# Kernel tuning notes

Measured on AMD Instinct MI355X. Metric: run time of the kernel, lower is better.

The kernel has to match this reference:

```python
import jax, jax.numpy as jnp
import numpy as np

B, S, D = 2, 4096, 256
H, DH, DM = 8, 32, 1024
ROPE_BASE = 10000.0
LN_EPS = 1e-5


def _layer_norm(x, g, b):
    mu = jnp.mean(x, axis=-1, keepdims=True)
    var = jnp.mean(jnp.square(x - mu), axis=-1, keepdims=True)
    return (x - mu) * jax.lax.rsqrt(var + LN_EPS) * g + b


def _rope(x):
    # x: [b, s, h, d_head]; lucidrains interleaved-pair RoPE
    s, d = x.shape[1], x.shape[-1]
    inv_freq = 1.0 / (ROPE_BASE ** (jnp.arange(0, d, 2, dtype=jnp.float32) / d))  # [d/2]
    freqs = jnp.arange(s, dtype=jnp.float32)[:, None] * inv_freq[None, :]          # [s, d/2]
    freqs = jnp.repeat(freqs, 2, axis=-1)                                          # [s, d]
    cos = jnp.cos(freqs)[None, :, None, :]
    sin = jnp.sin(freqs)[None, :, None, :]
    x1, x2 = x[..., 0::2], x[..., 1::2]
    rot = jnp.stack((-x2, x1), axis=-1).reshape(x.shape)
    return x * cos + rot * sin


def setup_inputs() -> dict:
    key = jax.random.key(0)
    ks = jax.random.split(key, 8)
    sw = 1.0 / np.sqrt(D)
    return {
        "x": jax.random.normal(ks[0], (B, S, D), jnp.float32),
        "Wq": jax.random.normal(ks[1], (D, D), jnp.float32) * sw,
        "Wk": jax.random.normal(ks[2], (D, D), jnp.float32) * sw,
        "Wv": jax.random.normal(ks[3], (D, D), jnp.float32) * sw,
        "Wo": jax.random.normal(ks[4], (D, D), jnp.float32) * sw,
        "ln1_g": jnp.ones((D,), jnp.float32),
        "ln1_b": jnp.zeros((D,), jnp.float32),
        "ln2_g": jnp.ones((D,), jnp.float32),
        "ln2_b": jnp.zeros((D,), jnp.float32),
        "W2": jax.random.normal(ks[5], (DM, D), jnp.float32) * sw,
        "b2": jnp.zeros((DM,), jnp.float32),
        "W3": jax.random.normal(ks[6], (D, DM), jnp.float32) * (1.0 / np.sqrt(DM)),
        "b3": jnp.zeros((D,), jnp.float32),
    }


def reference(x, Wq, Wk, Wv, Wo, ln1_g, ln1_b, ln2_g, ln2_b, W2, b2, W3, b3):
    b, s, d = x.shape
    h, dh = H, DH
    xn = _layer_norm(x, ln1_g, ln1_b)
    q = (xn @ Wq.T).reshape(b, s, h, dh)
    k = (xn @ Wk.T).reshape(b, s, h, dh)
    v = (xn @ Wv.T).reshape(b, s, h, dh)
    q = _rope(q)
    k = _rope(k)
    # scores: [b, h, q, k] (full matrix, matching original implementation)
    scores = jnp.einsum('bqhd,bkhd->bhqk', q, k) / np.sqrt(dh)
    attn = jax.nn.softmax(scores, axis=-1)
    out = jnp.einsum('bhqk,bkhd->bqhd', attn, v).reshape(b, s, d)
    out = out @ Wo.T
    mlp_in = out + x
    y = _layer_norm(mlp_in, ln2_g, ln2_b)
    y = jax.nn.gelu(y @ W2.T + b2, approximate=False)
    y = y @ W3.T + b3
    return y + mlp_in
```

## Files before the change

### kernel.cpp

```cpp
#include <hip/hip_runtime.h>
#include <math.h>

#define D 256
#define S 4096
#define H 8
#define DH 32
#define DM 1024
#define NTOK 8192

typedef __attribute__((ext_vector_type(8))) short short8;
typedef __attribute__((ext_vector_type(4))) float f32x4;

#define QSCALE (0.17677669529663687f * 1.4426950408889634f)

__device__ inline unsigned short f2bf(float f) {
    union { float f; unsigned u; } v; v.f = f;
    unsigned r = v.u + 0x7fffu + ((v.u >> 16) & 1u);
    return (unsigned short)(r >> 16);
}
__device__ inline void gload16(const void* g, void* l) {
    __builtin_amdgcn_global_load_lds((const __attribute__((address_space(1))) void*)g,
                                     (__attribute__((address_space(3))) void*)l, 16, 0, 0);
}

__global__ void conv_all(const float* __restrict__ Wq, const float* __restrict__ Wk,
                         const float* __restrict__ Wv, const float* __restrict__ Wo,
                         const float* __restrict__ W2, const float* __restrict__ W3,
                         unsigned short* __restrict__ wqkv, unsigned short* __restrict__ wo_b,
                         unsigned short* __restrict__ w2_b, unsigned short* __restrict__ w3_b,
                         float* __restrict__ ct, float* __restrict__ st) {
    int i = blockIdx.x * 256 + threadIdx.x;
    if (i < 196608) {
        const float* s = (i < 65536) ? Wq : ((i < 131072) ? Wk : Wv);
        wqkv[i] = f2bf(s[i & 65535]);
    } else if (i < 262144) {
        wo_b[i - 196608] = f2bf(Wo[i - 196608]);
    } else if (i < 524288) {
        w2_b[i - 262144] = f2bf(W2[i - 262144]);
    } else if (i < 786432) {
        w3_b[i - 524288] = f2bf(W3[i - 524288]);
    } else {
        int j = i - 786432;
        int spos = j >> 4, pi = j & 15;
        float inv_freq = powf(10000.0f, -(float)(2 * pi) / 32.0f);
        float fr = (float)spos * inv_freq;
        ct[j] = cosf(fr);
        st[j] = sinf(fr);
    }
}

__global__ void ln_kernel(const float* __restrict__ x, const float* __restrict__ g,
                          const float* __restrict__ b, unsigned short* __restrict__ out) {
    __shared__ float red[8];
    int row = blockIdx.x;
    int tid = threadIdx.x;
    float v = x[(size_t)row * D + tid];
    float s = v, s2 = v * v;
    #pragma unroll
    for (int off = 32; off > 0; off >>= 1) {
        s  += __shfl_xor(s, off, 64);
        s2 += __shfl_xor(s2, off, 64);
    }
    int wave = tid >> 6;
    if ((tid & 63) == 0) { red[wave] = s; red[wave + 4] = s2; }
    __syncthreads();
    float sum   = red[0] + red[1] + red[2] + red[3];
    float sumsq = red[4] + red[5] + red[6] + red[7];
    float mu  = sum * (1.0f / D);
    float var = sumsq * (1.0f / D) - mu * mu;
    float rs  = rsqrtf(var + 1e-5f);
    out[(size_t)row * D + tid] = f2bf((v - mu) * rs * g[tid] + b[tid]);
}

__global__ __launch_bounds__(256) void gemm_fat(const unsigned short* __restrict__ A,
        const unsigned short* __restrict__ Bw, void* __restrict__ outp,
        unsigned short* __restrict__ vt,
        const float* __restrict__ bias, const float* __restrict__ res,
        const float* __restrict__ ct, const float* __restrict__ st,
        int N, int K, int mode) {
    __shared__ unsigned short As[64 * 256];
    __shared__ unsigned short Bs[64 * 256];
    int tid = threadIdx.x;
    int w = tid >> 6, l = tid & 63;
    int lm = l & 15, lg = l >> 4;
    int wm = (w >> 1) * 32, wn = (w & 1) * 32;
    int bm = blockIdx.x * 64, bn = blockIdx.y * 64;
    int row0 = tid >> 5, pc = tid & 31;
    int pcx = (pc ^ (row0 & 7)) * 8;
    const int swz = lm & 7;
    f32x4 acc[2][2] = {};

    for (int kp = 0; kp < K; kp += 256) {
        if (kp) __syncthreads();
        const unsigned short* Ag = A + (size_t)(bm + row0) * K + kp + pcx;
        const unsigned short* Bg = Bw + (size_t)(bn + row0) * K + kp + pcx;
        unsigned short* al = &As[w * 512];
        unsigned short* bl = &Bs[w * 512];
        #pragma unroll
        for (int it = 0; it < 8; ++it) {
            gload16(Ag + (size_t)it * 8 * K, al + it * 2048);
            gload16(Bg + (size_t)it * 8 * K, bl + it * 2048);
        }
        __syncthreads();
        #pragma unroll
        for (int kk = 0; kk < 8; ++kk) {
            short8 af[2], bf[2];
            int ch = ((kk * 4 + lg) ^ swz) * 8;
            #pragma unroll
            for (int i = 0; i < 2; ++i) af[i] = *(const short8*)&As[(wm + i * 16 + lm) * 256 + ch];
            #pragma unroll
            for (int i = 0; i < 2; ++i) bf[i] = *(const short8*)&Bs[(wn + i * 16 + lm) * 256 + ch];
            #pragma unroll
            for (int mi = 0; mi < 2; ++mi)
                #pragma unroll
                for (int ni = 0; ni < 2; ++ni)
                    acc[mi][ni] = __builtin_amdgcn_mfma_f32_16x16x32_bf16(af[mi], bf[ni], acc[mi][ni], 0, 0, 0);
        }
    }

    if (mode == 0) {
        if (bn >= 512) {
            #pragma unroll
            for (int mi = 0; mi < 2; ++mi) {
                #pragma unroll
                for (int ni = 0; ni < 2; ++ni) {
                    int ng = bn + wn + ni * 16 + lm - 512;
                    int hh = ng >> 5, dh = ng & 31;
                    int mg0 = bm + wm + mi * 16 + lg * 4;
                    int bb = mg0 >> 12, ss = mg0 & 4095;
                    ushort4 pv;
                    pv.x = f2bf(acc[mi][ni][0]); pv.y = f2bf(acc[mi][ni][1]);
                    pv.z = f2bf(acc[mi][ni][2]); pv.w = f2bf(acc[mi][ni][3]);
                    *(ushort4*)(vt + ((size_t)((bb * 8 + hh) * 32 + dh)) * S + ss) = pv;
                }
            }
        } else {
            #pragma unroll
            for (int mi = 0; mi < 2; ++mi) {
                #pragma unroll
                for (int ni = 0; ni < 2; ++ni) {
                    int ng = bn + wn + ni * 16 + lm;
                    int pi = (ng & 31) >> 1;
                    float sgn = (ng & 1) ? 1.f : -1.f;
                    float qs  = (ng < 256) ? QSCALE : 1.f;
                    #pragma unroll
                    for (int r2 = 0; r2 < 4; ++r2) {
                        int mg = bm + wm + mi * 16 + lg * 4 + r2;
                        int spos = mg & (S - 1);
                        float vv = acc[mi][ni][r2];
                        float pv = __shfl_xor(vv, 1, 64);
                        float cs = ct[spos * 16 + pi];
                        float sn = st[spos * 16 + pi];
                        float ov = (vv * cs + sgn * pv * sn) * qs;
                        ((unsigned short*)outp)[(size_t)mg * N + ng] = f2bf(ov);
                    }
                }
            }
        }
        return;
    }
    #pragma unroll
    for (int mi = 0; mi < 2; ++mi) {
        #pragma unroll
        for (int ni = 0; ni < 2; ++ni) {
            int ng = bn + wn + ni * 16 + lm;
            #pragma unroll
            for (int r2 = 0; r2 < 4; ++r2) {
                int mg = bm + wm + mi * 16 + lg * 4 + r2;
                float v = acc[mi][ni][r2];
                size_t idx = (size_t)mg * N + ng;
                if (mode == 1) {
                    ((float*)outp)[idx] = v + res[idx];
                } else if (mode == 2) {
                    float t = v + bias[ng];
                    ((unsigned short*)outp)[idx] = f2bf(0.5f * t * (1.0f + erff(t * 0.70710678118654752f)));
                } else {
                    ((float*)outp)[idx] = v + bias[ng] + res[idx];
                }
            }
        }
    }
}

__global__ __launch_bounds__(512) void attn_kernel(const unsigned short* __restrict__ Cq,
        const unsigned short* __restrict__ vt, unsigned short* __restrict__ out) {
    __shared__ unsigned short Ks[2][64][32];
    __shared__ unsigned short Vs[2][32][64];
    __shared__ unsigned short Ones[16][64];
    int tid = threadIdx.x;
    int w = tid >> 6, l = tid & 63;
    int lm = l & 15, lg = l >> 4;
    int qt = blockIdx.x & 31;
    int bh = blockIdx.x >> 5;
    int b = bh >> 3, h = bh & 7;
    int q0 = qt * 128 + w * 16;

    if (tid < 256) {
        unsigned short val = (tid < 16) ? (unsigned short)0x3F80 : (unsigned short)0;
        *(ushort4*)(&Ones[0][0] + tid * 4) = make_ushort4(val, val, val, val);
    }

    const short8 qf = *(const short8*)(Cq + ((size_t)(b * S + q0 + lm)) * 768 + h * DH + lg * 8);
    int ws = w & 3;
    int p = ws * 16 + (l >> 2);
    int krow = ((p >> 5) << 5) + (((p >> 2) & 3) << 3) + (((p >> 4) & 1) << 2) + (p & 3);
    const unsigned short* kg = Cq + ((size_t)(b * S)) * 768 + 256 + h * 32
                               + (size_t)krow * 768 + ((l & 3) ^ ((l >> 3) & 3)) * 8;
    const unsigned short* vg = vt + ((size_t)(bh * 32 + ws * 8 + (l >> 3))) * S + ((l & 7) ^ (l >> 3)) * 8;
    unsigned short* klds0 = &Ks[0][ws * 16][0];
    unsigned short* vlds0 = &Vs[0][ws * 8][0];
    unsigned short* klds1 = &Ks[1][ws * 16][0];
    unsigned short* vlds1 = &Vs[1][ws * 8][0];
    const int kswz = (lm >> 1) & 3;
    const int vswz = lm & 7;

    f32x4 o0 = {0.f, 0.f, 0.f, 0.f}, o1 = {0.f, 0.f, 0.f, 0.f}, o2 = {0.f, 0.f, 0.f, 0.f};
    const f32x4 z = {0.f, 0.f, 0.f, 0.f};

    if (w < 4) gload16(kg, klds0);
    else       gload16(vg, vlds0);

    #pragma unroll 2
    for (int it = 0; it < S / 64; ++it) {
        int cur = it & 1;
        __syncthreads();
        if (it + 1 < S / 64) {
            if (w < 4) gload16(kg + (size_t)(it + 1) * 64 * 768, cur ? klds0 : klds1);
            else       gload16(vg + (size_t)(it + 1) * 64,       cur ? vlds0 : vlds1);
        }
        #pragma unroll
        for (int half = 0; half < 2; ++half) {
            short8 kf0 = *(const short8*)&Ks[cur][half * 32 + lm][(lg ^ kswz) * 8];
            short8 kf1 = *(const short8*)&Ks[cur][half * 32 + 16 + lm][(lg ^ kswz) * 8];
            f32x4 s0 = __builtin_amdgcn_mfma_f32_16x16x32_bf16(kf0, qf, z, 0, 0, 0);
            f32x4 s1 = __builtin_amdgcn_mfma_f32_16x16x32_bf16(kf1, qf, z, 0, 0, 0);
            unsigned u0[4], u1[4];
            #pragma unroll
            for (int i = 0; i < 4; ++i) {
                union { float f; unsigned u; } c0, c1;
                c0.f = __builtin_amdgcn_exp2f(s0[i]);
                c1.f = __builtin_amdgcn_exp2f(s1[i]);
                u0[i] = c0.u;
                u1[i] = c1.u;
            }
            union { unsigned u[4]; short8 s; } pk;
            pk.u[0] = __builtin_amdgcn_perm(u0[1], u0[0], 0x07060302u);
            pk.u[1] = __builtin_amdgcn_perm(u0[3], u0[2], 0x07060302u);
            pk.u[2] = __builtin_amdgcn_perm(u1[1], u1[0], 0x07060302u);
            pk.u[3] = __builtin_amdgcn_perm(u1[3], u1[2], 0x07060302u);
            short8 pf = pk.s;
            int vc = ((half * 4 + lg) ^ vswz) * 8;
            short8 va0 = *(const short8*)&Vs[cur][lm][vc];
            short8 va1 = *(const short8*)&Vs[cur][16 + lm][vc];
            short8 va2 = *(const short8*)&Ones[lm][vc];
            o0 = __builtin_amdgcn_mfma_f32_16x16x32_bf16(va0, pf, o0, 0, 0, 0);
            o1 = __builtin_amdgcn_mfma_f32_16x16x32_bf16(va1, pf, o1, 0, 0, 0);
            o2 = __builtin_amdgcn_mfma_f32_16x16x32_bf16(va2, pf, o2, 0, 0, 0);
        }
    }
    float lsum = __shfl(o2[0], lm, 64);
    float inv = 1.0f / lsum;
    ushort4 r0, r1;
    r0.x = f2bf(o0[0] * inv); r0.y = f2bf(o0[1] * inv);
    r0.z = f2bf(o0[2] * inv); r0.w = f2bf(o0[3] * inv);
    r1.x = f2bf(o1[0] * inv); r1.y = f2bf(o1[1] * inv);
    r1.z = f2bf(o1[2] * inv); r1.w = f2bf(o1[3] * inv);
    unsigned short* ob = out + ((size_t)(b * S + q0 + lm)) * D + h * DH;
    *(ushort4*)(ob + lg * 4)      = r0;
    *(ushort4*)(ob + 16 + lg * 4) = r1;
}

extern "C" void kernel_launch(void* const* d_in, const int* in_sizes, int n_in,
                              void* d_out, int out_size, void* d_ws, size_t ws_size,
                              hipStream_t stream) {
    const float* x     = (const float*)d_in[0];
    const float* Wq    = (const float*)d_in[1];
    const float* Wk    = (const float*)d_in[2];
    const float* Wv    = (const float*)d_in[3];
    const float* Wo    = (const float*)d_in[4];
    const float* ln1_g = (const float*)d_in[5];
    const float* ln1_b = (const float*)d_in[6];
    const float* ln2_g = (const float*)d_in[7];
    const float* ln2_b = (const float*)d_in[8];
    const float* W2    = (const float*)d_in[9];
    const float* b2    = (const float*)d_in[10];
    const float* W3    = (const float*)d_in[11];
    const float* b3    = (const float*)d_in[12];

    char* w8 = (char*)d_ws;
    unsigned short* wqkv = (unsigned short*)(w8);
    unsigned short* wo_b = (unsigned short*)(w8 + 393216);
    unsigned short* w2_b = (unsigned short*)(w8 + 524288);
    unsigned short* w3_b = (unsigned short*)(w8 + 1048576);
    float*          ct   = (float*)(w8 + 1572864);
    float*          st   = (float*)(w8 + 1835008);
    unsigned short* xn   = (unsigned short*)(w8 + 2097152);
    unsigned short* Cq   = (unsigned short*)(w8 + 6291456);
    unsigned short* hb   = Cq;
    unsigned short* vtb  = (unsigned short*)(w8 + 23068672);
    unsigned short* ab   = (unsigned short*)(w8 + 27262976);
    float*          mlpin= (float*)(w8 + 31457280);
    unsigned short* yn   = xn;

    conv_all<<<3328, 256, 0, stream>>>(Wq, Wk, Wv, Wo, W2, W3, wqkv, wo_b, w2_b, w3_b, ct, st);
    ln_kernel<<<NTOK, 256, 0, stream>>>(x, ln1_g, ln1_b, xn);
    gemm_fat<<<dim3(128, 12), 256, 0, stream>>>(xn, wqkv, Cq, vtb, nullptr, nullptr, ct, st, 768, 256, 0);
    attn_kernel<<<512, 512, 0, stream>>>(Cq, vtb, ab);
    gemm_fat<<<dim3(128, 4), 256, 0, stream>>>(ab, wo_b, mlpin, nullptr, nullptr, x, nullptr, nullptr, 256, 256, 1);
    ln_kernel<<<NTOK, 256, 0, stream>>>(mlpin, ln2_g, ln2_b, yn);
    gemm_fat<<<dim3(128, 16), 256, 0, stream>>>(yn, w2_b, hb, nullptr, b2, nullptr, nullptr, nullptr, 1024, 256, 2);
    gemm_fat<<<dim3(128, 4), 256, 0, stream>>>(hb, w3_b, (float*)d_out, nullptr, b3, mlpin, nullptr, nullptr, 256, 1024, 3);
}
```

Measured before the change: 206.2 us.

## Split attention keys across two wave groups and load GEMM weights into registers

The attention kernel now gives 64 queries to each block and splits the key range between two groups of four waves. Each group double-buffers its own K/V tiles, and the partial outputs and denominators are combined through shared memory at the end. This doubles the block count to 1024, for more parallelism and fewer sequential iterations per wave. Separately, the GEMM loads B-operand fragments straight from global memory into registers instead of staging them in LDS. This halves LDS use, but adds register pressure and uncoalesced-ish global loads.

```diff
diff --git a/kernel.cpp b/kernel.cpp
--- a/kernel.cpp
+++ b/kernel.cpp
@@ -72,14 +72,13 @@
     out[(size_t)row * D + tid] = f2bf((v - mu) * rs * g[tid] + b[tid]);
 }
 
-__global__ __launch_bounds__(256) void gemm_fat(const unsigned short* __restrict__ A,
+__global__ __launch_bounds__(256) void gemm3(const unsigned short* __restrict__ A,
         const unsigned short* __restrict__ Bw, void* __restrict__ outp,
         unsigned short* __restrict__ vt,
         const float* __restrict__ bias, const float* __restrict__ res,
         const float* __restrict__ ct, const float* __restrict__ st,
         int N, int K, int mode) {
     __shared__ unsigned short As[64 * 256];
-    __shared__ unsigned short Bs[64 * 256];
     int tid = threadIdx.x;
     int w = tid >> 6, l = tid & 63;
     int lm = l & 15, lg = l >> 4;
@@ -93,28 +92,30 @@
     for (int kp = 0; kp < K; kp += 256) {
         if (kp) __syncthreads();
         const unsigned short* Ag = A + (size_t)(bm + row0) * K + kp + pcx;
-        const unsigned short* Bg = Bw + (size_t)(bn + row0) * K + kp + pcx;
         unsigned short* al = &As[w * 512];
-        unsigned short* bl = &Bs[w * 512];
-        #pragma unroll
-        for (int it = 0; it < 8; ++it) {
+        #pragma unroll
+        for (int it = 0; it < 8; ++it)
             gload16(Ag + (size_t)it * 8 * K, al + it * 2048);
-            gload16(Bg + (size_t)it * 8 * K, bl + it * 2048);
-        }
+        short8 breg[2][8];
+        const unsigned short* Bg = Bw + (size_t)(bn + wn + lm) * K + kp + lg * 8;
+        #pragma unroll
+        for (int ni = 0; ni < 2; ++ni)
+            #pragma unroll
+            for (int kk = 0; kk < 8; ++kk)
+                breg[ni][kk] = *(const short8*)(Bg + (size_t)(ni * 16) * K + kk * 32);
         __syncthreads();
         #pragma unroll
         for (int kk = 0; kk < 8; ++kk) {
-            short8 af[2], bf[2];
+            short8 af[2];
             int ch = ((kk * 4 + lg) ^ swz) * 8;
             #pragma unroll
-            for (int i = 0; i < 2; ++i) af[i] = *(const short8*)&As[(wm + i * 16 + lm) * 256 + ch];
-            #pragma unroll
-            for (int i = 0; i < 2; ++i) bf[i] = *(const short8*)&Bs[(wn + i * 16 + lm) * 256 + ch];
+            for (int i = 0; i < 2; ++i)
+                af[i] = *(const short8*)&As[(wm + i * 16 + lm) * 256 + ch];
             #pragma unroll
             for (int mi = 0; mi < 2; ++mi)
                 #pragma unroll
                 for (int ni = 0; ni < 2; ++ni)
-                    acc[mi][ni] = __builtin_amdgcn_mfma_f32_16x16x32_bf16(af[mi], bf[ni], acc[mi][ni], 0, 0, 0);
+                    acc[mi][ni] = __builtin_amdgcn_mfma_f32_16x16x32_bf16(af[mi], breg[ni][kk], acc[mi][ni], 0, 0, 0);
         }
     }
 
@@ -184,54 +185,51 @@
 
 __global__ __launch_bounds__(512) void attn_kernel(const unsigned short* __restrict__ Cq,
         const unsigned short* __restrict__ vt, unsigned short* __restrict__ out) {
-    __shared__ unsigned short Ks[2][64][32];
-    __shared__ unsigned short Vs[2][32][64];
+    __shared__ unsigned short Ks[2][2][64][32];
+    __shared__ unsigned short Vs[2][2][32][64];
     __shared__ unsigned short Ones[16][64];
     int tid = threadIdx.x;
     int w = tid >> 6, l = tid & 63;
+    int grp = w >> 2, ws = w & 3;
     int lm = l & 15, lg = l >> 4;
-    int qt = blockIdx.x & 31;
-    int bh = blockIdx.x >> 5;
-    int b = bh >> 3, h = bh & 7;
-    int q0 = qt * 128 + w * 16;
+    int qt = blockIdx.x & 63;
+    int bh = blockIdx.x >> 6;
+    int bb = bh >> 3, h = bh & 7;
+    int q0 = qt * 64 + ws * 16;
 
     if (tid < 256) {
         unsigned short val = (tid < 16) ? (unsigned short)0x3F80 : (unsigned short)0;
         *(ushort4*)(&Ones[0][0] + tid * 4) = make_ushort4(val, val, val, val);
     }
 
-    const short8 qf = *(const short8*)(Cq + ((size_t)(b * S + q0 + lm)) * 768 + h * DH + lg * 8);
-    int ws = w & 3;
+    const short8 qf = *(const short8*)(Cq + ((size_t)(bb * S + q0 + lm)) * 768 + h * DH + lg * 8);
     int p = ws * 16 + (l >> 2);
     int krow = ((p >> 5) << 5) + (((p >> 2) & 3) << 3) + (((p >> 4) & 1) << 2) + (p & 3);
-    const unsigned short* kg = Cq + ((size_t)(b * S)) * 768 + 256 + h * 32
+    const unsigned short* kg = Cq + ((size_t)(bb * S)) * 768 + 256 + h * 32
                                + (size_t)krow * 768 + ((l & 3) ^ ((l >> 3) & 3)) * 8;
     const unsigned short* vg = vt + ((size_t)(bh * 32 + ws * 8 + (l >> 3))) * S + ((l & 7) ^ (l >> 3)) * 8;
-    unsigned short* klds0 = &Ks[0][ws * 16][0];
-    unsigned short* vlds0 = &Vs[0][ws * 8][0];
-    unsigned short* klds1 = &Ks[1][ws * 16][0];
-    unsigned short* vlds1 = &Vs[1][ws * 8][0];
     const int kswz = (lm >> 1) & 3;
     const int vswz = lm & 7;
 
     f32x4 o0 = {0.f, 0.f, 0.f, 0.f}, o1 = {0.f, 0.f, 0.f, 0.f}, o2 = {0.f, 0.f, 0.f, 0.f};
     const f32x4 z = {0.f, 0.f, 0.f, 0.f};
 
-    if (w < 4) gload16(kg, klds0);
-    else       gload16(vg, vlds0);
+    gload16(kg + (size_t)grp * 64 * 768, &Ks[grp][0][ws * 16][0]);
+    gload16(vg + (size_t)grp * 64,       &Vs[grp][0][ws * 8][0]);
 
     #pragma unroll 2
-    for (int it = 0; it < S / 64; ++it) {
+    for (int it = 0; it < S / 128; ++it) {
         int cur = it & 1;
         __syncthreads();
-        if (it + 1 < S / 64) {
-            if (w < 4) gload16(kg + (size_t)(it + 1) * 64 * 768, cur ? klds0 : klds1);
-            else       gload16(vg + (size_t)(it + 1) * 64,       cur ? vlds0 : vlds1);
+        if (it + 1 < S / 128) {
+            size_t t = (size_t)(2 * (it + 1) + grp);
+            gload16(kg + t * 64 * 768, &Ks[grp][1 - cur][ws * 16][0]);
+            gload16(vg + t * 64,       &Vs[grp][1 - cur][ws * 8][0]);
         }
         #pragma unroll
         for (int half = 0; half < 2; ++half) {
-            short8 kf0 = *(const short8*)&Ks[cur][half * 32 + lm][(lg ^ kswz) * 8];
-            short8 kf1 = *(const short8*)&Ks[cur][half * 32 + 16 + lm][(lg ^ kswz) * 8];
+            short8 kf0 = *(const short8*)&Ks[grp][cur][half * 32 + lm][(lg ^ kswz) * 8];
+            short8 kf1 = *(const short8*)&Ks[grp][cur][half * 32 + 16 + lm][(lg ^ kswz) * 8];
             f32x4 s0 = __builtin_amdgcn_mfma_f32_16x16x32_bf16(kf0, qf, z, 0, 0, 0);
             f32x4 s1 = __builtin_amdgcn_mfma_f32_16x16x32_bf16(kf1, qf, z, 0, 0, 0);
             unsigned u0[4], u1[4];
@@ -250,24 +248,41 @@
             pk.u[3] = __builtin_amdgcn_perm(u1[3], u1[2], 0x07060302u);
             short8 pf = pk.s;
             int vc = ((half * 4 + lg) ^ vswz) * 8;
-            short8 va0 = *(const short8*)&Vs[cur][lm][vc];
-            short8 va1 = *(const short8*)&Vs[cur][16 + lm][vc];
+            short8 va0 = *(const short8*)&Vs[grp][cur][lm][vc];
+            short8 va1 = *(const short8*)&Vs[grp][cur][16 + lm][vc];
             short8 va2 = *(const short8*)&Ones[lm][vc];
             o0 = __builtin_amdgcn_mfma_f32_16x16x32_bf16(va0, pf, o0, 0, 0, 0);
             o1 = __builtin_amdgcn_mfma_f32_16x16x32_bf16(va1, pf, o1, 0, 0, 0);
             o2 = __builtin_amdgcn_mfma_f32_16x16x32_bf16(va2, pf, o2, 0, 0, 0);
         }
     }
-    float lsum = __shfl(o2[0], lm, 64);
-    float inv = 1.0f / lsum;
-    ushort4 r0, r1;
-    r0.x = f2bf(o0[0] * inv); r0.y = f2bf(o0[1] * inv);
-    r0.z = f2bf(o0[2] * inv); r0.w = f2bf(o0[3] * inv);
-    r1.x = f2bf(o1[0] * inv); r1.y = f2bf(o1[1] * inv);
-    r1.z = f2bf(o1[2] * inv); r1.w = f2bf(o1[3] * inv);
-    unsigned short* ob = out + ((size_t)(b * S + q0 + lm)) * D + h * DH;
-    *(ushort4*)(ob + lg * 4)      = r0;
-    *(ushort4*)(ob + 16 + lg * 4) = r1;
+    f32x4* Red0 = (f32x4*)&Ks[1][0][0][0];
+    f32x4* Red1 = (f32x4*)&Vs[1][0][0][0];
+    float* Den  = (float*)&Ones[0][0];
+    __syncthreads();
+    if (grp) {
+        Red0[ws * 64 + l] = o0;
+        Red1[ws * 64 + l] = o1;
+        Den[ws * 64 + l]  = o2[0];
+    }
+    __syncthreads();
+    if (!grp) {
+        f32x4 a0 = Red0[ws * 64 + l];
+        f32x4 a1 = Red1[ws * 64 + l];
+        float dd = o2[0] + Den[ws * 64 + l];
+        #pragma unroll
+        for (int i = 0; i < 4; ++i) { o0[i] += a0[i]; o1[i] += a1[i]; }
+        float lsum = __shfl(dd, lm, 64);
+        float inv = 1.0f / lsum;
+        ushort4 r0, r1;
+        r0.x = f2bf(o0[0] * inv); r0.y = f2bf(o0[1] * inv);
+        r0.z = f2bf(o0[2] * inv); r0.w = f2bf(o0[3] * inv);
+        r1.x = f2bf(o1[0] * inv); r1.y = f2bf(o1[1] * inv);
+        r1.z = f2bf(o1[2] * inv); r1.w = f2bf(o1[3] * inv);
+        unsigned short* ob = out + ((size_t)(bb * S + q0 + lm)) * D + h * DH;
+        *(ushort4*)(ob + lg * 4)      = r0;
+        *(ushort4*)(ob + 16 + lg * 4) = r1;
+    }
 }
 
 extern "C" void kernel_launch(void* const* d_in, const int* in_sizes, int n_in,
@@ -304,10 +319,10 @@
 
     conv_all<<<3328, 256, 0, stream>>>(Wq, Wk, Wv, Wo, W2, W3, wqkv, wo_b, w2_b, w3_b, ct, st);
     ln_kernel<<<NTOK, 256, 0, stream>>>(x, ln1_g, ln1_b, xn);
-    gemm_fat<<<dim3(128, 12), 256, 0, stream>>>(xn, wqkv, Cq, vtb, nullptr, nullptr, ct, st, 768, 256, 0);
-    attn_kernel<<<512, 512, 0, stream>>>(Cq, vtb, ab);
-    gemm_fat<<<dim3(128, 4), 256, 0, stream>>>(ab, wo_b, mlpin, nullptr, nullptr, x, nullptr, nullptr, 256, 256, 1);
+    gemm3<<<dim3(128, 12), 256, 0, stream>>>(xn, wqkv, Cq, vtb, nullptr, nullptr, ct, st, 768, 256, 0);
+    attn_kernel<<<1024, 512, 0, stream>>>(Cq, vtb, ab);
+    gemm3<<<dim3(128, 4), 256, 0, stream>>>(ab, wo_b, mlpin, nullptr, nullptr, x, nullptr, nullptr, 256, 256, 1);
     ln_kernel<<<NTOK, 256, 0, stream>>>(mlpin, ln2_g, ln2_b, yn);
-    gemm_fat<<<dim3(128, 16), 256, 0, stream>>>(yn, w2_b, hb, nullptr, b2, nullptr, nullptr, nullptr, 1024, 256, 2);
-    gemm_fat<<<dim3(128, 4), 256, 0, stream>>>(hb, w3_b, (float*)d_out, nullptr, b3, mlpin, nullptr, nullptr, 256, 1024, 3);
-}
+    gemm3<<<dim3(128, 16), 256, 0, stream>>>(yn, w2_b, hb, nullptr, b2, nullptr, nullptr, nullptr, 1024, 256, 2);
+    gemm3<<<dim3(128, 4), 256, 0, stream>>>(hb, w3_b, (float*)d_out, nullptr, b3, mlpin, nullptr, nullptr, 256, 1024, 3);
+}
```

Result: slower. 230.6 us (+11.9%).
